# Optimization experiments

Measured on AMD Instinct MI355X. Metric: run time of the kernel, lower is better.

Reference implementation:

```python
import jax, jax.numpy as jnp
import numpy as np

DIM_K = 128
MODEL_DIM = 1024
B, S = 8, 2048

def setup_inputs() -> dict:
    key = jax.random.key(0)
    k1, k2, k3, k4, k5, k6, k7 = jax.random.split(key, 7)
    return {
        "query": jax.random.normal(k1, (B, S, MODEL_DIM), dtype=jnp.float32),
        "key": jax.random.normal(k2, (B, S, MODEL_DIM), dtype=jnp.float32),
        "value": jax.random.normal(k3, (B, S, MODEL_DIM), dtype=jnp.float32),
        "mask": jax.random.randint(k4, (B, S, S), 0, 2, dtype=jnp.int32),
        # nn.Linear(model_dim, dim_k, bias=False): weight shape [dim_k, model_dim]
        "Wq": jax.random.normal(k5, (DIM_K, MODEL_DIM), dtype=jnp.float32) * (MODEL_DIM ** -0.5),
        "Wk": jax.random.normal(k6, (DIM_K, MODEL_DIM), dtype=jnp.float32) * (MODEL_DIM ** -0.5),
        "Wv": jax.random.normal(k7, (DIM_K, MODEL_DIM), dtype=jnp.float32) * (MODEL_DIM ** -0.5),
    }

def reference(query, key, value, mask, Wq, Wk, Wv):
    # projections: y = x @ W.T
    q = jnp.einsum('bsm,km->bsk', query, Wq)
    k = jnp.einsum('bsm,km->bsk', key, Wk)
    v = jnp.einsum('bsm,km->bsk', value, Wv)
    scale = 1.0 / jnp.sqrt(jnp.float32(DIM_K))
    pre_score = jnp.einsum('bqk,bsk->bqs', q, k) * scale  # [B,Sq,Sk]
    pre_score = jnp.where(mask == 0, jnp.float32(-1e9), pre_score)
    score = jax.nn.softmax(pre_score, axis=-1)
    return jnp.einsum('bqs,bsk->bqk', score, v)
```

## Files before the change

### kernel.cpp

```cpp
#include <hip/hip_runtime.h>
#include <hip/hip_fp16.h>

#define SEQ 2048
#define DMODEL 1024
#define DK 128

typedef _Float16 f16x8 __attribute__((ext_vector_type(8)));
typedef float    f32x4 __attribute__((ext_vector_type(4)));

#define L2E 1.44269504088896340736f

#define WS_Q  393216
#define WS_K  2490368
#define WS_VT 4587520
#define WS_F16_BYTES 13369344ull

__global__ __launch_bounds__(256) void wconv_kernel(
    const float* __restrict__ wq, const float* __restrict__ wk,
    const float* __restrict__ wv, _Float16* __restrict__ w16)
{
    int i = blockIdx.x * 256 + threadIdx.x;
    int p = i >> 17;
    int j = i & 131071;
    const float* src = (p == 0) ? wq : ((p == 1) ? wk : wv);
    float f = src[j];
    if (p == 0) f *= 0.08838834764831845f;
    w16[i] = (_Float16)f;
}

__global__ __launch_bounds__(128) void proj_kernel(
    const float* __restrict__ xq, const float* __restrict__ xk,
    const float* __restrict__ xv, const _Float16* __restrict__ w16,
    _Float16* __restrict__ qws, _Float16* __restrict__ kws, _Float16* __restrict__ vtws)
{
    const int p = blockIdx.y;
    const float* __restrict__ x = (p == 0) ? xq : ((p == 1) ? xk : xv);
    const _Float16* __restrict__ w = w16 + p * 131072;

    const int mtile = blockIdx.x;
    const int m0 = mtile << 6;
    const int t = threadIdx.x;
    const int wv_ = t >> 6;
    const int lane = t & 63;
    const int l15 = lane & 15, g = lane >> 4;
    const int mw = m0 + wv_ * 32;

    f32x4 acc[2][8];
#pragma unroll
    for (int mi = 0; mi < 2; ++mi)
#pragma unroll
        for (int nt = 0; nt < 8; ++nt) acc[mi][nt] = (f32x4){0.f, 0.f, 0.f, 0.f};

    const float* x0 = x + (size_t)(mw + l15) * 1024 + g * 8;
    const float* x1 = x0 + 16 * 1024;
    const _Float16* wb = w + (size_t)l15 * 1024 + g * 8;

#pragma unroll 2
    for (int ks = 0; ks < 32; ++ks) {
        const int col = ks * 32;
        f32x4 a00 = *(const f32x4*)(x0 + col);
        f32x4 a01 = *(const f32x4*)(x0 + col + 4);
        f32x4 a10 = *(const f32x4*)(x1 + col);
        f32x4 a11 = *(const f32x4*)(x1 + col + 4);
        f16x8 af0, af1;
#pragma unroll
        for (int j = 0; j < 4; ++j) {
            af0[j]     = (_Float16)a00[j];
            af0[4 + j] = (_Float16)a01[j];
            af1[j]     = (_Float16)a10[j];
            af1[4 + j] = (_Float16)a11[j];
        }
#pragma unroll
        for (int nt = 0; nt < 8; ++nt) {
            f16x8 bf = *(const f16x8*)(wb + (size_t)nt * 16 * 1024 + col);
            acc[0][nt] = __builtin_amdgcn_mfma_f32_16x16x32_f16(af0, bf, acc[0][nt], 0, 0, 0);
            acc[1][nt] = __builtin_amdgcn_mfma_f32_16x16x32_f16(af1, bf, acc[1][nt], 0, 0, 0);
        }
    }

    __shared__ __align__(16) _Float16 olds[9216];
#pragma unroll
    for (int mi = 0; mi < 2; ++mi)
#pragma unroll
        for (int nt = 0; nt < 8; ++nt)
#pragma unroll
            for (int r = 0; r < 4; ++r) {
                int rowl = wv_ * 32 + mi * 16 + g * 4 + r;
                int col = nt * 16 + l15;
                _Float16 v = (_Float16)acc[mi][nt][r];
                if (p < 2) olds[rowl * 136 + col] = v;
                else       olds[col * 72 + rowl] = v;
            }
    __syncthreads();

    if (p < 2) {
#pragma unroll
        for (int i = 0; i < 8; ++i) {
            int idx = i * 128 + t;
            int row = idx >> 4, ck = idx & 15;
            f16x8 v = *(const f16x8*)(olds + row * 136 + ck * 8);
            _Float16* dst = ((p == 0) ? qws : kws) + (size_t)(m0 + row) * 128 + ck * 8;
            *(f16x8*)dst = v;
        }
    } else {
        const int bq = mtile >> 5, s0 = (mtile & 31) << 6;
#pragma unroll
        for (int i = 0; i < 8; ++i) {
            int idx = i * 128 + t;
            int row = idx >> 3, ck = idx & 7;
            f16x8 v = *(const f16x8*)(olds + row * 72 + ck * 8);
            _Float16* dst = vtws + ((size_t)(bq * 128 + row)) * 2048 + s0 + ck * 8;
            *(f16x8*)dst = v;
        }
    }
}

__global__ __launch_bounds__(256) void flash_kernel(
    const _Float16* __restrict__ qws, const _Float16* __restrict__ kws,
    const _Float16* __restrict__ vtws, const int* __restrict__ mask,
    float* __restrict__ out, float* __restrict__ part, float* __restrict__ mlbuf,
    int ktp)
{
    const int bb = blockIdx.x & 7;
    const int rest = blockIdx.x >> 3;
    const int mtile = rest & 31;
    const int jsplit = rest >> 5;
    const int sq0 = mtile << 6;
    const int t = threadIdx.x;
    const int wv_ = t >> 6;
    const int lane = t & 63;
    const int l15 = lane & 15, g = lane >> 4;

    __shared__ __align__(16) _Float16 smem[22528];
    _Float16* klds = smem;
    _Float16* vtlds = smem + 8704;
    _Float16* plds = smem + 17920 + wv_ * 1152;

    f16x8 qf[4];
    {
        const _Float16* qp = qws + ((size_t)(bb * 2048 + sq0 + wv_ * 16 + l15)) * 128 + g * 8;
#pragma unroll
        for (int ks = 0; ks < 4; ++ks) qf[ks] = *(const f16x8*)(qp + ks * 32);
    }

    f32x4 o[8];
#pragma unroll
    for (int nt = 0; nt < 8; ++nt) o[nt] = (f32x4){0.f, 0.f, 0.f, 0.f};
    float m_run[4], l_run[4];
#pragma unroll
    for (int r = 0; r < 4; ++r) { m_run[r] = -__builtin_inff(); l_run[r] = 0.f; }

    const int* mbase = mask + ((size_t)(bb * 2048 + sq0 + wv_ * 16 + g * 4)) * 2048 + l15;

    const int kt_begin = jsplit * ktp, kt_end = kt_begin + ktp;
    for (int kt = kt_begin; kt < kt_end; ++kt) {
        const int n0 = kt << 6;
        __syncthreads();
#pragma unroll
        for (int i = 0; i < 8; ++i) {
            int idx = i * 256 + t;
            if (idx < 1024) {
                int row = idx >> 4, ck = idx & 15;
                *(f16x8*)(klds + row * 136 + ck * 8) =
                    *(const f16x8*)(kws + ((size_t)(bb * 2048 + n0 + row)) * 128 + ck * 8);
            } else {
                int v = idx - 1024;
                int row = v >> 3, ck = v & 7;
                *(f16x8*)(vtlds + row * 72 + ck * 8) =
                    *(const f16x8*)(vtws + ((size_t)(bb * 128 + row)) * 2048 + n0 + ck * 8);
            }
        }
        __syncthreads();

        int mv[4][4];
#pragma unroll
        for (int nt = 0; nt < 4; ++nt)
#pragma unroll
            for (int r = 0; r < 4; ++r)
                mv[nt][r] = mbase[(size_t)r * 2048 + n0 + nt * 16];

        f32x4 sf[4];
#pragma unroll
        for (int nt = 0; nt < 4; ++nt) sf[nt] = (f32x4){0.f, 0.f, 0.f, 0.f};
#pragma unroll
        for (int nt = 0; nt < 4; ++nt) {
            const _Float16* kp = klds + (nt * 16 + l15) * 136 + g * 8;
#pragma unroll
            for (int ks = 0; ks < 4; ++ks) {
                f16x8 bfk = *(const f16x8*)(kp + ks * 32);
                sf[nt] = __builtin_amdgcn_mfma_f32_16x16x32_f16(qf[ks], bfk, sf[nt], 0, 0, 0);
            }
        }

        float mx[4], mnew[4], alpha[4], psum[4];
#pragma unroll
        for (int r = 0; r < 4; ++r)
            mx[r] = fmaxf(fmaxf(sf[0][r], sf[1][r]), fmaxf(sf[2][r], sf[3][r]));
#pragma unroll
        for (int off = 1; off < 16; off <<= 1)
#pragma unroll
            for (int r = 0; r < 4; ++r)
                mx[r] = fmaxf(mx[r], __shfl_xor(mx[r], off, 64));
#pragma unroll
        for (int r = 0; r < 4; ++r) {
            mnew[r] = fmaxf(m_run[r], mx[r]);
            alpha[r] = exp2f((m_run[r] - mnew[r]) * L2E);
            psum[r] = 0.f;
        }
#pragma unroll
        for (int nt = 0; nt < 4; ++nt)
#pragma unroll
            for (int r = 0; r < 4; ++r) {
                float pv = exp2f((sf[nt][r] - mnew[r]) * L2E);
                pv = mv[nt][r] ? pv : 0.f;
                psum[r] += pv;
                plds[(g * 4 + r) * 72 + nt * 16 + l15] = (_Float16)pv;
            }
#pragma unroll
        for (int off = 1; off < 16; off <<= 1)
#pragma unroll
            for (int r = 0; r < 4; ++r)
                psum[r] += __shfl_xor(psum[r], off, 64);
#pragma unroll
        for (int r = 0; r < 4; ++r) {
            l_run[r] = l_run[r] * alpha[r] + psum[r];
            m_run[r] = mnew[r];
        }
#pragma unroll
        for (int nt = 0; nt < 8; ++nt)
#pragma unroll
            for (int r = 0; r < 4; ++r) o[nt][r] *= alpha[r];

        f16x8 pa[2];
#pragma unroll
        for (int ks2 = 0; ks2 < 2; ++ks2)
            pa[ks2] = *(const f16x8*)(plds + l15 * 72 + ks2 * 32 + g * 8);

#pragma unroll
        for (int nt2 = 0; nt2 < 8; ++nt2) {
            const _Float16* vp = vtlds + (nt2 * 16 + l15) * 72 + g * 8;
#pragma unroll
            for (int ks2 = 0; ks2 < 2; ++ks2) {
                f16x8 bfv = *(const f16x8*)(vp + ks2 * 32);
                o[nt2] = __builtin_amdgcn_mfma_f32_16x16x32_f16(pa[ks2], bfv, o[nt2], 0, 0, 0);
            }
        }
    }

    if (part == nullptr) {
        float inv[4];
#pragma unroll
        for (int r = 0; r < 4; ++r) inv[r] = 1.0f / l_run[r];
#pragma unroll
        for (int nt2 = 0; nt2 < 8; ++nt2)
#pragma unroll
            for (int r = 0; r < 4; ++r)
                out[((size_t)(bb * 2048 + sq0 + wv_ * 16 + g * 4 + r)) * 128 + nt2 * 16 + l15] =
                    o[nt2][r] * inv[r];
    } else {
#pragma unroll
        for (int nt2 = 0; nt2 < 8; ++nt2)
#pragma unroll
            for (int r = 0; r < 4; ++r) {
                size_t rowg = (size_t)(bb * 2048 + sq0 + wv_ * 16 + g * 4 + r);
                part[((size_t)jsplit * 16384 + rowg) * 128 + nt2 * 16 + l15] = o[nt2][r];
            }
        if (l15 == 0) {
#pragma unroll
            for (int r = 0; r < 4; ++r) {
                size_t rowg = (size_t)(bb * 2048 + sq0 + wv_ * 16 + g * 4 + r);
                mlbuf[((size_t)jsplit * 16384 + rowg) * 2]     = m_run[r];
                mlbuf[((size_t)jsplit * 16384 + rowg) * 2 + 1] = l_run[r];
            }
        }
    }
}

__global__ __launch_bounds__(256) void merge_kernel(
    const float* __restrict__ part, const float* __restrict__ mlbuf,
    float* __restrict__ out, int J)
{
    int t = threadIdx.x;
    size_t row = (size_t)blockIdx.x * 8 + (t >> 5);
    int c = (t & 31) * 4;
    float mj[4];
    float m = -__builtin_inff();
    for (int j = 0; j < J; ++j) {
        mj[j] = mlbuf[((size_t)j * 16384 + row) * 2];
        m = fmaxf(m, mj[j]);
    }
    float l = 0.f;
    f32x4 acc = (f32x4){0.f, 0.f, 0.f, 0.f};
    for (int j = 0; j < J; ++j) {
        float w = exp2f((mj[j] - m) * L2E);
        l += w * mlbuf[((size_t)j * 16384 + row) * 2 + 1];
        f32x4 v = *(const f32x4*)(part + ((size_t)j * 16384 + row) * 128 + c);
#pragma unroll
        for (int e = 0; e < 4; ++e) acc[e] += w * v[e];
    }
    float inv = 1.0f / l;
#pragma unroll
    for (int e = 0; e < 4; ++e) acc[e] *= inv;
    *(f32x4*)(out + row * 128 + c) = acc;
}

extern "C" void kernel_launch(void* const* d_in, const int* in_sizes, int n_in,
                              void* d_out, int out_size, void* d_ws, size_t ws_size,
                              hipStream_t stream)
{
    const float* query = (const float*)d_in[0];
    const float* key   = (const float*)d_in[1];
    const float* value = (const float*)d_in[2];
    const int*   mask  = (const int*)d_in[3];
    const float* Wq    = (const float*)d_in[4];
    const float* Wk    = (const float*)d_in[5];
    const float* Wv    = (const float*)d_in[6];
    float* out = (float*)d_out;

    _Float16* w16 = (_Float16*)d_ws;
    _Float16* qws = w16 + WS_Q;
    _Float16* kws = w16 + WS_K;
    _Float16* vtws = w16 + WS_VT;

    const size_t per_split = 16384ull * 128 * 4 + 16384ull * 8;
    int J = 1;
    if (ws_size >= WS_F16_BYTES + 4 * per_split)      J = 4;
    else if (ws_size >= WS_F16_BYTES + 2 * per_split) J = 2;
    float* part = (J > 1) ? (float*)((char*)d_ws + WS_F16_BYTES) : nullptr;
    float* mlbuf = (J > 1) ? (part + (size_t)J * 16384 * 128) : nullptr;

    wconv_kernel<<<1536, 256, 0, stream>>>(Wq, Wk, Wv, w16);
    proj_kernel<<<dim3(256, 3), 128, 0, stream>>>(query, key, value, w16, qws, kws, vtws);
    flash_kernel<<<256 * J, 256, 0, stream>>>(qws, kws, vtws, mask, out, part, mlbuf, 32 / J);
    if (J > 1) merge_kernel<<<2048, 256, 0, stream>>>(part, mlbuf, out, J);
}
```

Baseline: 395.8 us.

## Use four waves per projection block with register double-buffered loads

The projection kernel now runs 256 threads per block, with each wave owning 16 rows instead of 32. This doubles the number of waves in flight to hide global-load latency. The k-loop is software-pipelined: activation and weight fragments for the next step are loaded into a second register set while MFMAs run on the current one. The cost is that each block reads the weight fragments twice as often per row computed, and the extra buffers raise register pressure.

```diff
diff --git a/kernel.cpp b/kernel.cpp
--- a/kernel.cpp
+++ b/kernel.cpp
@@ -28,7 +28,7 @@
     w16[i] = (_Float16)f;
 }
 
-__global__ __launch_bounds__(128) void proj_kernel(
+__global__ __launch_bounds__(256) void proj_kernel(
     const float* __restrict__ xq, const float* __restrict__ xk,
     const float* __restrict__ xv, const _Float16* __restrict__ w16,
     _Float16* __restrict__ qws, _Float16* __restrict__ kws, _Float16* __restrict__ vtws)
@@ -43,60 +43,67 @@
     const int wv_ = t >> 6;
     const int lane = t & 63;
     const int l15 = lane & 15, g = lane >> 4;
-    const int mw = m0 + wv_ * 32;
-
-    f32x4 acc[2][8];
-#pragma unroll
-    for (int mi = 0; mi < 2; ++mi)
-#pragma unroll
-        for (int nt = 0; nt < 8; ++nt) acc[mi][nt] = (f32x4){0.f, 0.f, 0.f, 0.f};
+    const int mw = m0 + wv_ * 16;
+
+    f32x4 acc[8];
+#pragma unroll
+    for (int nt = 0; nt < 8; ++nt) acc[nt] = (f32x4){0.f, 0.f, 0.f, 0.f};
 
     const float* x0 = x + (size_t)(mw + l15) * 1024 + g * 8;
-    const float* x1 = x0 + 16 * 1024;
     const _Float16* wb = w + (size_t)l15 * 1024 + g * 8;
 
-#pragma unroll 2
-    for (int ks = 0; ks < 32; ++ks) {
-        const int col = ks * 32;
-        f32x4 a00 = *(const f32x4*)(x0 + col);
-        f32x4 a01 = *(const f32x4*)(x0 + col + 4);
-        f32x4 a10 = *(const f32x4*)(x1 + col);
-        f32x4 a11 = *(const f32x4*)(x1 + col + 4);
-        f16x8 af0, af1;
-#pragma unroll
-        for (int j = 0; j < 4; ++j) {
-            af0[j]     = (_Float16)a00[j];
-            af0[4 + j] = (_Float16)a01[j];
-            af1[j]     = (_Float16)a10[j];
-            af1[4 + j] = (_Float16)a11[j];
-        }
-#pragma unroll
-        for (int nt = 0; nt < 8; ++nt) {
-            f16x8 bf = *(const f16x8*)(wb + (size_t)nt * 16 * 1024 + col);
-            acc[0][nt] = __builtin_amdgcn_mfma_f32_16x16x32_f16(af0, bf, acc[0][nt], 0, 0, 0);
-            acc[1][nt] = __builtin_amdgcn_mfma_f32_16x16x32_f16(af1, bf, acc[1][nt], 0, 0, 0);
-        }
+    f32x4 a0 = *(const f32x4*)(x0);
+    f32x4 a1 = *(const f32x4*)(x0 + 4);
+    f16x8 bA[8], bB[8];
+#pragma unroll
+    for (int nt = 0; nt < 8; ++nt)
+        bA[nt] = *(const f16x8*)(wb + (size_t)nt * 16384);
+
+    for (int ks = 0; ks < 32; ks += 2) {
+        f32x4 a2 = *(const f32x4*)(x0 + ks * 32 + 32);
+        f32x4 a3 = *(const f32x4*)(x0 + ks * 32 + 36);
+#pragma unroll
+        for (int nt = 0; nt < 8; ++nt)
+            bB[nt] = *(const f16x8*)(wb + (size_t)nt * 16384 + ks * 32 + 32);
+        f16x8 af;
+#pragma unroll
+        for (int j = 0; j < 4; ++j) { af[j] = (_Float16)a0[j]; af[4 + j] = (_Float16)a1[j]; }
+#pragma unroll
+        for (int nt = 0; nt < 8; ++nt)
+            acc[nt] = __builtin_amdgcn_mfma_f32_16x16x32_f16(af, bA[nt], acc[nt], 0, 0, 0);
+
+        if (ks + 2 < 32) {
+            a0 = *(const f32x4*)(x0 + ks * 32 + 64);
+            a1 = *(const f32x4*)(x0 + ks * 32 + 68);
+#pragma unroll
+            for (int nt = 0; nt < 8; ++nt)
+                bA[nt] = *(const f16x8*)(wb + (size_t)nt * 16384 + ks * 32 + 64);
+        }
+        f16x8 ag;
+#pragma unroll
+        for (int j = 0; j < 4; ++j) { ag[j] = (_Float16)a2[j]; ag[4 + j] = (_Float16)a3[j]; }
+#pragma unroll
+        for (int nt = 0; nt < 8; ++nt)
+            acc[nt] = __builtin_amdgcn_mfma_f32_16x16x32_f16(ag, bB[nt], acc[nt], 0, 0, 0);
     }
 
     __shared__ __align__(16) _Float16 olds[9216];
 #pragma unroll
-    for (int mi = 0; mi < 2; ++mi)
-#pragma unroll
-        for (int nt = 0; nt < 8; ++nt)
-#pragma unroll
-            for (int r = 0; r < 4; ++r) {
-                int rowl = wv_ * 32 + mi * 16 + g * 4 + r;
-                int col = nt * 16 + l15;
-                _Float16 v = (_Float16)acc[mi][nt][r];
-                if (p < 2) olds[rowl * 136 + col] = v;
-                else       olds[col * 72 + rowl] = v;
-            }
+    for (int nt = 0; nt < 8; ++nt)
+#pragma unroll
+        for (int r = 0; r < 4; ++r) {
+            int rowl = wv_ * 16 + g * 4 + r;
+            int col = nt * 16 + l15;
+            _Float16 v = (_Float16)acc[nt][r];
+            if (p < 2) olds[rowl * 136 + col] = v;
+            else       olds[col * 72 + rowl] = v;
+        }
     __syncthreads();
 
     if (p < 2) {
 #pragma unroll
-        for (int i = 0; i < 8; ++i) {
-            int idx = i * 128 + t;
+        for (int i = 0; i < 4; ++i) {
+            int idx = i * 256 + t;
             int row = idx >> 4, ck = idx & 15;
             f16x8 v = *(const f16x8*)(olds + row * 136 + ck * 8);
             _Float16* dst = ((p == 0) ? qws : kws) + (size_t)(m0 + row) * 128 + ck * 8;
@@ -105,8 +112,8 @@
     } else {
         const int bq = mtile >> 5, s0 = (mtile & 31) << 6;
 #pragma unroll
-        for (int i = 0; i < 8; ++i) {
-            int idx = i * 128 + t;
+        for (int i = 0; i < 4; ++i) {
+            int idx = i * 256 + t;
             int row = idx >> 3, ck = idx & 7;
             f16x8 v = *(const f16x8*)(olds + row * 72 + ck * 8);
             _Float16* dst = vtws + ((size_t)(bq * 128 + row)) * 2048 + s0 + ck * 8;
@@ -330,7 +337,7 @@
     float* mlbuf = (J > 1) ? (part + (size_t)J * 16384 * 128) : nullptr;
 
     wconv_kernel<<<1536, 256, 0, stream>>>(Wq, Wk, Wv, w16);
-    proj_kernel<<<dim3(256, 3), 128, 0, stream>>>(query, key, value, w16, qws, kws, vtws);
+    proj_kernel<<<dim3(256, 3), 256, 0, stream>>>(query, key, value, w16, qws, kws, vtws);
     flash_kernel<<<256 * J, 256, 0, stream>>>(qws, kws, vtws, mask, out, part, mlbuf, 32 / J);
     if (J > 1) merge_kernel<<<2048, 256, 0, stream>>>(part, mlbuf, out, J);
 }
```

Result: slower. 449.6 us (+13.6%).
